# Performance work log

Hardware: AMD Instinct MI355X
Metric: run time of the kernel (lower is better)

The kernel has to match this reference:

```python
import jax, jax.numpy as jnp
import numpy as np
import math

V, D, H, KVH, L, T, B = 32000, 1024, 16, 4, 4, 2048, 2
HD = D // H            # head_dim = 64
GROUP = H // KVH       # GQA group size = 4
KVW = KVH * HD         # kv width = 256
EPS = 1e-5


def _alibi_slopes(n_heads):
    # n_heads=16 is a power of two
    start = 2.0 ** (-2.0 ** (-(math.log2(n_heads) - 3)))
    return np.array([start * start ** i for i in range(n_heads)], dtype=np.float32)


def setup_inputs() -> dict:
    key = jax.random.key(0)
    ks = jax.random.split(key, 8)
    s = 0.02
    inp = {
        "tok_emb": jax.random.normal(ks[0], (V, D), jnp.float32) * s,
        "ln1_s": jnp.ones((L, D), jnp.float32),
        "ln1_b": jnp.zeros((L, D), jnp.float32),
        "qkv_w": jax.random.normal(ks[1], (L, D, D + 2 * KVW), jnp.float32) * s,
        "qkv_b": jnp.zeros((L, D + 2 * KVW), jnp.float32),
        "proj_w": jax.random.normal(ks[2], (L, D, D), jnp.float32) * s,
        "proj_b": jnp.zeros((L, D), jnp.float32),
        "ln2_s": jnp.ones((L, D), jnp.float32),
        "ln2_b": jnp.zeros((L, D), jnp.float32),
        "fc1_w": jax.random.normal(ks[3], (L, D, 4 * D), jnp.float32) * s,
        "fc1_b": jnp.zeros((L, 4 * D), jnp.float32),
        "fc2_w": jax.random.normal(ks[4], (L, 4 * D, D), jnp.float32) * s,
        "fc2_b": jnp.zeros((L, D), jnp.float32),
        "lnf_s": jnp.ones((D,), jnp.float32),
        "lnf_b": jnp.zeros((D,), jnp.float32),
        "idx": jax.random.randint(ks[5], (B, T), 0, V, jnp.int32),
    }
    return inp


def _ln(x, s, b):
    mu = jnp.mean(x, axis=-1, keepdims=True)
    var = jnp.var(x, axis=-1, keepdims=True)
    return (x - mu) * jax.lax.rsqrt(var + EPS) * s + b


def _forward(tok_emb, ln1_s, ln1_b, qkv_w, qkv_b, proj_w, proj_b,
             ln2_s, ln2_b, fc1_w, fc1_b, fc2_w, fc2_b, lnf_s, lnf_b, idx):
    x = tok_emb[idx]  # (B, T, D); ALiBi => no learned positional embedding

    # combined causal mask + ALiBi bias: (1, H, T, T)
    slopes = jnp.asarray(_alibi_slopes(H)).reshape(1, H, 1, 1)
    pos = jnp.arange(T, dtype=jnp.float32)
    rel = jnp.minimum(pos[None, :] - pos[:, None], 0.0)  # (T, T), clamp_max(0)
    causal = pos[None, :] <= pos[:, None]
    bias = jnp.where(causal[None, None], rel[None, None] * slopes, -jnp.inf)

    scale = 1.0 / math.sqrt(HD)
    for l in range(L):
        h = _ln(x, ln1_s[l], ln1_b[l])
        qkv = h @ qkv_w[l] + qkv_b[l]
        q = qkv[..., :D].reshape(B, T, H, HD).transpose(0, 2, 1, 3)
        k = qkv[..., D:D + KVW].reshape(B, T, KVH, HD).transpose(0, 2, 1, 3)
        v = qkv[..., D + KVW:].reshape(B, T, KVH, HD).transpose(0, 2, 1, 3)
        k = jnp.repeat(k, GROUP, axis=1)  # GQA broadcast -> (B, H, T, HD)
        v = jnp.repeat(v, GROUP, axis=1)
        att = jnp.einsum("bhqd,bhkd->bhqk", q, k) * scale + bias
        att = jax.nn.softmax(att, axis=-1)
        o = jnp.einsum("bhqk,bhkd->bhqd", att, v)
        o = o.transpose(0, 2, 1, 3).reshape(B, T, D)
        x = x + o @ proj_w[l] + proj_b[l]
        h = _ln(x, ln2_s[l], ln2_b[l])
        x = x + jax.nn.gelu(h @ fc1_w[l] + fc1_b[l], approximate=False) @ fc2_w[l] + fc2_b[l]

    x = _ln(x, lnf_s, lnf_b)
    logits = x @ tok_emb.T  # tied head (no bias)
    return logits


def reference(tok_emb, ln1_s, ln1_b, qkv_w, qkv_b, proj_w, proj_b,
              ln2_s, ln2_b, fc1_w, fc1_b, fc2_w, fc2_b, lnf_s, lnf_b, idx):
    return _forward(tok_emb, ln1_s, ln1_b, qkv_w, qkv_b, proj_w, proj_b,
                    ln2_s, ln2_b, fc1_w, fc1_b, fc2_w, fc2_b, lnf_s, lnf_b, idx)
```

## Files before the change

### kernel.cpp

```cpp
#include <hip/hip_runtime.h>

#define DEV __device__ __forceinline__
typedef unsigned short u16;
typedef __bf16 bf16_t;
typedef bf16_t bf16x8 __attribute__((ext_vector_type(8)));
typedef float f32x4 __attribute__((ext_vector_type(4)));

DEV u16 f2bf(float f){ unsigned u=__float_as_uint(f); return (u16)((u + 0x7fffu + ((u>>16)&1u))>>16); }

DEV void gl_lds16(const void* g, void* l){
  __builtin_amdgcn_global_load_lds((__attribute__((address_space(1))) void*)g,
                                   (__attribute__((address_space(3))) void*)l, 16, 0, 0);
}
DEV f32x4 MFMA(bf16x8 a, bf16x8 b, f32x4 c){
  return __builtin_amdgcn_mfma_f32_16x16x32_bf16(a, b, c, 0, 0, 0);
}
DEV bf16x8 ld8(const u16* p){ return *(const bf16x8*)p; }

__global__ __launch_bounds__(256) void k_embed(const int* __restrict__ idx,
                                               const float* __restrict__ emb,
                                               float* __restrict__ x){
  int row = blockIdx.x;
  int tok = idx[row];
  const float4* s = (const float4*)(emb + (size_t)tok*1024);
  float4* d = (float4*)(x + (size_t)row*1024);
  d[threadIdx.x] = s[threadIdx.x];
}

__global__ __launch_bounds__(256) void k_ln(const float* __restrict__ x,
                                            const float* __restrict__ sc,
                                            const float* __restrict__ bi,
                                            u16* __restrict__ out){
  int row = blockIdx.x;
  const float* xr = x + (size_t)row*1024;
  float4 v = ((const float4*)xr)[threadIdx.x];
  float s = v.x+v.y+v.z+v.w;
  float q = v.x*v.x+v.y*v.y+v.z*v.z+v.w*v.w;
  #pragma unroll
  for(int m=1;m<64;m<<=1){ s += __shfl_xor(s,m); q += __shfl_xor(q,m); }
  __shared__ float ss[4], sq[4];
  int w = threadIdx.x>>6;
  if((threadIdx.x&63)==0){ ss[w]=s; sq[w]=q; }
  __syncthreads();
  s = ss[0]+ss[1]+ss[2]+ss[3];
  q = sq[0]+sq[1]+sq[2]+sq[3];
  float mu = s*(1.f/1024.f);
  float var = q*(1.f/1024.f) - mu*mu;
  float rs = rsqrtf(var + 1e-5f);
  float4 sv = ((const float4*)sc)[threadIdx.x];
  float4 bv = ((const float4*)bi)[threadIdx.x];
  ushort4 o;
  o.x = f2bf((v.x-mu)*rs*sv.x + bv.x);
  o.y = f2bf((v.y-mu)*rs*sv.y + bv.y);
  o.z = f2bf((v.z-mu)*rs*sv.z + bv.z);
  o.w = f2bf((v.w-mu)*rs*sv.w + bv.w);
  *(ushort4*)(out + (size_t)row*1024 + threadIdx.x*4) = o;
}

__global__ __launch_bounds__(256) void k_convT(const float* __restrict__ W,
                                               u16* __restrict__ Wt, int K, int N){
  __shared__ float tile[64][68];
  size_t loff = (size_t)blockIdx.z * K * N;
  W  += loff;  Wt += loff;
  int n0 = blockIdx.x*64, k0 = blockIdx.y*64;
  int tx = threadIdx.x & 15, ty = threadIdx.x >> 4;
  #pragma unroll
  for(int r=0;r<4;r++){
    int row = ty + r*16;
    float4 v = *(const float4*)&W[(size_t)(k0+row)*N + n0 + tx*4];
    *(float4*)&tile[row][tx*4] = v;
  }
  __syncthreads();
  int nn = threadIdx.x >> 2, kq = threadIdx.x & 3;
  #pragma unroll
  for(int r=0;r<4;r++){
    int k = (kq + r*4)*4;
    ushort4 o;
    o.x = f2bf(tile[k+0][nn]); o.y = f2bf(tile[k+1][nn]);
    o.z = f2bf(tile[k+2][nn]); o.w = f2bf(tile[k+3][nn]);
    *(ushort4*)&Wt[(size_t)(n0+nn)*K + k0 + k] = o;
  }
}

__global__ __launch_bounds__(256) void k_conv(const float* __restrict__ in,
                                              u16* __restrict__ out, int n4){
  int i = blockIdx.x*256 + threadIdx.x;
  if(i < n4){
    float4 v = ((const float4*)in)[i];
    ushort4 o; o.x=f2bf(v.x); o.y=f2bf(v.y); o.z=f2bf(v.z); o.w=f2bf(v.w);
    ((ushort4*)out)[i] = o;
  }
}

template<int EPI, int SWAP>
__global__ __launch_bounds__(256) void k_gemm(const u16* __restrict__ A,
                                              const u16* __restrict__ Bt,
                                              const float* __restrict__ bias,
                                              void* __restrict__ out,
                                              float* __restrict__ res,
                                              int M, int N, int K, int m_base){
  __shared__ __align__(16) u16 As[128*64];
  __shared__ __align__(16) u16 Bs[128*64];
  int t = threadIdx.x, l = t & 63, w = t >> 6;
  int g = l >> 4, lr = l & 15;
  int wr = w >> 1, wc = w & 1;
  int m0, n0;
  if constexpr(SWAP){ m0 = m_base + blockIdx.x*128; n0 = blockIdx.y*128; }
  else              { m0 = m_base + blockIdx.y*128; n0 = blockIdx.x*128; }
  f32x4 acc[4][4];
  #pragma unroll
  for(int i=0;i<4;i++)
    #pragma unroll
    for(int j=0;j<4;j++) acc[i][j] = f32x4{0.f,0.f,0.f,0.f};

  int sr = t >> 3;
  int sc = (((t & 7) ^ (sr & 7)) * 8);
  const u16* pa = A  + (size_t)(m0 + sr)*K + sc;
  const u16* pb = Bt + (size_t)(n0 + sr)*K + sc;
  u16* lda = As + t*8;
  u16* ldb = Bs + t*8;
  const int rs_a = (lr & 7)*8;

  for(int k0=0; k0<K; k0+=64){
    #pragma unroll
    for(int i=0;i<4;i++){
      gl_lds16(pa + (size_t)(i*32)*K, lda + i*2048);
      gl_lds16(pb + (size_t)(i*32)*K, ldb + i*2048);
    }
    pa += 64; pb += 64;
    __syncthreads();
    bf16x8 af[4][2], bfr[4][2];
    #pragma unroll
    for(int mi=0;mi<4;mi++){
      int row = wr*64 + mi*16 + lr;
      af[mi][0] = ld8(&As[row*64 + ((g*8     ) ^ rs_a)]);
      af[mi][1] = ld8(&As[row*64 + ((g*8 + 32) ^ rs_a)]);
    }
    #pragma unroll
    for(int ni=0;ni<4;ni++){
      int row = wc*64 + ni*16 + lr;
      bfr[ni][0] = ld8(&Bs[row*64 + ((g*8     ) ^ rs_a)]);
      bfr[ni][1] = ld8(&Bs[row*64 + ((g*8 + 32) ^ rs_a)]);
    }
    #pragma unroll
    for(int mi=0;mi<4;mi++)
      #pragma unroll
      for(int ni=0;ni<4;ni++){
        acc[mi][ni] = MFMA(af[mi][0], bfr[ni][0], acc[mi][ni]);
        acc[mi][ni] = MFMA(af[mi][1], bfr[ni][1], acc[mi][ni]);
      }
    __syncthreads();
  }

  float bv[4];
  #pragma unroll
  for(int ni=0;ni<4;ni++){
    if constexpr(EPI==3) bv[ni] = 0.f;
    else bv[ni] = bias[n0 + wc*64 + ni*16 + lr];
  }
  #pragma unroll
  for(int mi=0;mi<4;mi++){
    int row = m0 + wr*64 + mi*16 + g*4;
    #pragma unroll
    for(int ni=0;ni<4;ni++){
      int col = n0 + wc*64 + ni*16 + lr;
      #pragma unroll
      for(int r=0;r<4;r++){
        float v = acc[mi][ni][r] + bv[ni];
        size_t oidx = (size_t)(row + r)*N + col;
        if constexpr(EPI==0){
          ((u16*)out)[oidx] = f2bf(v);
        } else if constexpr(EPI==1){
          res[oidx] += v;
        } else if constexpr(EPI==2){
          float gv = 0.5f*v*(1.f + erff(v*0.70710678118654752f));
          ((u16*)out)[oidx] = f2bf(gv);
        } else {
          ((float*)out)[oidx] = v;
        }
      }
    }
  }
}

__global__ __launch_bounds__(256) void k_gemm_n64(const u16* __restrict__ A,
                                                  const u16* __restrict__ Bt,
                                                  const float* __restrict__ bias,
                                                  float* __restrict__ res,
                                                  int M, int N, int K){
  __shared__ __align__(16) u16 As[128*64];
  __shared__ __align__(16) u16 Bs[64*64];
  int t = threadIdx.x, l = t & 63, w = t >> 6;
  int g = l >> 4, lr = l & 15;
  int wr = w >> 1, wc = w & 1;
  int m0 = blockIdx.y*128, n0 = blockIdx.x*64;
  f32x4 acc[4][2];
  #pragma unroll
  for(int i=0;i<4;i++)
    #pragma unroll
    for(int j=0;j<2;j++) acc[i][j] = f32x4{0.f,0.f,0.f,0.f};

  int sr = t >> 3;
  int sc = (((t & 7) ^ (sr & 7)) * 8);
  const u16* pa = A  + (size_t)(m0 + sr)*K + sc;
  const u16* pb = Bt + (size_t)(n0 + sr)*K + sc;
  u16* lda = As + t*8;
  u16* ldb = Bs + t*8;
  const int rs_a = (lr & 7)*8;

  for(int k0=0; k0<K; k0+=64){
    #pragma unroll
    for(int i=0;i<4;i++)
      gl_lds16(pa + (size_t)(i*32)*K, lda + i*2048);
    #pragma unroll
    for(int i=0;i<2;i++)
      gl_lds16(pb + (size_t)(i*32)*K, ldb + i*2048);
    pa += 64; pb += 64;
    __syncthreads();
    bf16x8 af[4][2], bfr[2][2];
    #pragma unroll
    for(int mi=0;mi<4;mi++){
      int row = wr*64 + mi*16 + lr;
      af[mi][0] = ld8(&As[row*64 + ((g*8     ) ^ rs_a)]);
      af[mi][1] = ld8(&As[row*64 + ((g*8 + 32) ^ rs_a)]);
    }
    #pragma unroll
    for(int ni=0;ni<2;ni++){
      int row = wc*32 + ni*16 + lr;
      bfr[ni][0] = ld8(&Bs[row*64 + ((g*8     ) ^ rs_a)]);
      bfr[ni][1] = ld8(&Bs[row*64 + ((g*8 + 32) ^ rs_a)]);
    }
    #pragma unroll
    for(int mi=0;mi<4;mi++)
      #pragma unroll
      for(int ni=0;ni<2;ni++){
        acc[mi][ni] = MFMA(af[mi][0], bfr[ni][0], acc[mi][ni]);
        acc[mi][ni] = MFMA(af[mi][1], bfr[ni][1], acc[mi][ni]);
      }
    __syncthreads();
  }

  float bv[2];
  #pragma unroll
  for(int ni=0;ni<2;ni++) bv[ni] = bias[n0 + wc*32 + ni*16 + lr];
  #pragma unroll
  for(int mi=0;mi<4;mi++){
    int row = m0 + wr*64 + mi*16 + g*4;
    #pragma unroll
    for(int ni=0;ni<2;ni++){
      int col = n0 + wc*32 + ni*16 + lr;
      #pragma unroll
      for(int r=0;r<4;r++)
        res[(size_t)(row + r)*N + col] += acc[mi][ni][r] + bv[ni];
    }
  }
}

__global__ __launch_bounds__(512) void k_gemm256(const u16* __restrict__ A,
                                                 const u16* __restrict__ Bt,
                                                 float* __restrict__ out,
                                                 int M, int N, int K, int m_base){
  __shared__ __align__(16) u16 As[2][256*64];
  __shared__ __align__(16) u16 Bs[2][256*64];
  int t = threadIdx.x, l = t & 63, wid = t >> 6;
  int g = l >> 4, lr = l & 15;
  int m0 = m_base + blockIdx.x*256, n0 = blockIdx.y*256;
  f32x4 acc[2][16];
  #pragma unroll
  for(int mi=0;mi<2;mi++)
    #pragma unroll
    for(int i=0;i<16;i++) acc[mi][i] = f32x4{0.f,0.f,0.f,0.f};

  int srow = t >> 3;
  int scol = ((t & 7) ^ (srow & 7)) * 8;
  const int rs = (lr & 7) * 8;
  int nt = K >> 6;

  auto stage_half = [&](int jj, int h){
    int buf = jj & 1; int k0s = jj << 6;
    if(h < 2){
      #pragma unroll
      for(int c=0;c<2;c++){
        int rr = h*128 + c*64 + srow;
        gl_lds16(A + (size_t)(m0 + rr)*K + k0s + scol,
                 &As[buf][rr*64 + (t&7)*8]);
      }
    } else {
      #pragma unroll
      for(int c=0;c<2;c++){
        int rr = (h-2)*128 + c*64 + srow;
        gl_lds16(Bt + (size_t)(n0 + rr)*K + k0s + scol,
                 &Bs[buf][rr*64 + (t&7)*8]);
      }
    }
  };

  stage_half(0,0); stage_half(0,1); stage_half(0,2); stage_half(0,3);
  asm volatile("s_waitcnt vmcnt(2)" ::: "memory");
  __builtin_amdgcn_s_barrier();
  __builtin_amdgcn_sched_barrier(0);

  bf16x8 af[2][2];
  for(int j=0; j<nt; ++j){
    const u16* Ab = As[j & 1];
    const u16* Bb = Bs[j & 1];
    bool pf = (j + 1 < nt);
    #pragma unroll
    for(int q=0; q<4; ++q){
      if(q == 0){
        #pragma unroll
        for(int mi=0;mi<2;mi++){
          int row = wid*32 + mi*16 + lr;
          af[mi][0] = ld8(&Ab[row*64 + ((g*8     ) ^ rs)]);
          af[mi][1] = ld8(&Ab[row*64 + ((g*8 + 32) ^ rs)]);
        }
      }
      bf16x8 bfr[4][2];
      #pragma unroll
      for(int i=0;i<4;i++){
        int row = (q*4 + i)*16 + lr;
        bfr[i][0] = ld8(&Bb[row*64 + ((g*8     ) ^ rs)]);
        bfr[i][1] = ld8(&Bb[row*64 + ((g*8 + 32) ^ rs)]);
      }
      if(pf) stage_half(j+1, q);
      __builtin_amdgcn_s_barrier();
      __builtin_amdgcn_sched_barrier(0);
      __builtin_amdgcn_s_setprio(1);
      #pragma unroll
      for(int mi=0;mi<2;mi++)
        #pragma unroll
        for(int i=0;i<4;i++){
          acc[mi][q*4+i] = MFMA(af[mi][0], bfr[i][0], acc[mi][q*4+i]);
          acc[mi][q*4+i] = MFMA(af[mi][1], bfr[i][1], acc[mi][q*4+i]);
        }
      __builtin_amdgcn_s_setprio(0);
      if(q == 1) asm volatile("s_waitcnt vmcnt(4)" ::: "memory");
      if(q == 3) asm volatile("s_waitcnt vmcnt(2)" ::: "memory");
      __builtin_amdgcn_s_barrier();
      __builtin_amdgcn_sched_barrier(0);
    }
  }

  #pragma unroll
  for(int mi=0;mi<2;mi++){
    int row = m0 + wid*32 + mi*16 + g*4;
    #pragma unroll
    for(int i=0;i<16;i++){
      int col = n0 + i*16 + lr;
      #pragma unroll
      for(int r=0;r<4;r++)
        out[(size_t)(row + r)*N + col] = acc[mi][i][r];
    }
  }
}

__global__ __launch_bounds__(256) void k_gemm_f32b(const u16* __restrict__ A,
                                                   const float* __restrict__ B,
                                                   float* __restrict__ out,
                                                   int M, int N, int K, int m_base){
  __shared__ __align__(16) u16 As[128*32];
  __shared__ __align__(16) u16 Bs[128*32];
  int t = threadIdx.x, l = t & 63, w = t >> 6;
  int g = l >> 4, lr = l & 15;
  int wr = w >> 1, wc = w & 1;
  int m0 = m_base + blockIdx.y*128, n0 = blockIdx.x*128;
  f32x4 acc[4][4];
  #pragma unroll
  for(int i=0;i<4;i++)
    #pragma unroll
    for(int j=0;j<4;j++) acc[i][j] = f32x4{0.f,0.f,0.f,0.f};

  int r0 = t >> 2, c0 = (t & 3)*8;
  const u16* pa0 = A + (size_t)(m0 + r0)*K + c0;
  const u16* pa1 = A + (size_t)(m0 + r0 + 64)*K + c0;
  u16* la0 = As + t*8;  u16* la1 = As + (t+256)*8;
  int br = t >> 1, bc = (t & 1)*16;
  const float* pb = B + (size_t)(n0 + br)*K + bc;

  for(int k0=0; k0<K; k0+=32){
    gl_lds16(pa0, la0); gl_lds16(pa1, la1);
    pa0 += 32; pa1 += 32;
    float4 f0 = ((const float4*)pb)[0];
    float4 f1 = ((const float4*)pb)[1];
    float4 f2 = ((const float4*)pb)[2];
    float4 f3 = ((const float4*)pb)[3];
    pb += 32;
    ushort4 u0{f2bf(f0.x),f2bf(f0.y),f2bf(f0.z),f2bf(f0.w)};
    ushort4 u1{f2bf(f1.x),f2bf(f1.y),f2bf(f1.z),f2bf(f1.w)};
    ushort4 u2{f2bf(f2.x),f2bf(f2.y),f2bf(f2.z),f2bf(f2.w)};
    ushort4 u3{f2bf(f3.x),f2bf(f3.y),f2bf(f3.z),f2bf(f3.w)};
    *(ushort4*)&Bs[br*32 + bc +  0] = u0;
    *(ushort4*)&Bs[br*32 + bc +  4] = u1;
    *(ushort4*)&Bs[br*32 + bc +  8] = u2;
    *(ushort4*)&Bs[br*32 + bc + 12] = u3;
    __syncthreads();
    bf16x8 af[4], bfr[4];
    #pragma unroll
    for(int mi=0;mi<4;mi++) af[mi]  = ld8(&As[(wr*64 + mi*16 + lr)*32 + g*8]);
    #pragma unroll
    for(int ni=0;ni<4;ni++) bfr[ni] = ld8(&Bs[(wc*64 + ni*16 + lr)*32 + g*8]);
    #pragma unroll
    for(int mi=0;mi<4;mi++)
      #pragma unroll
      for(int ni=0;ni<4;ni++)
        acc[mi][ni] = MFMA(af[mi], bfr[ni], acc[mi][ni]);
    __syncthreads();
  }

  #pragma unroll
  for(int mi=0;mi<4;mi++){
    int row = m0 + wr*64 + mi*16 + g*4;
    #pragma unroll
    for(int ni=0;ni<4;ni++){
      int col = n0 + wc*64 + ni*16 + lr;
      #pragma unroll
      for(int r=0;r<4;r++)
        out[(size_t)(row + r)*N + col] = acc[mi][ni][r];
    }
  }
}

__global__ __launch_bounds__(512) void k_attn(const u16* __restrict__ qkv,
                                              u16* __restrict__ atto){
  __shared__ __align__(16) u16 Ksm[64*72];
  __shared__ __align__(16) u16 Vsm[64*72];
  __shared__ __align__(16) u16 Psm[8][16*72];
  int t = threadIdx.x, l = t & 63, w = t >> 6, g = l >> 4, lr = l & 15;
  int bh = blockIdx.y; int b = bh >> 4, h = bh & 15, kvh = h >> 2;
  int qb = blockIdx.x * 128;
  const float L2E = 1.44269504088896f;
  const float C1  = 0.125f * L2E;
  float slopeL = exp2f(-0.5f*(float)(h+1)) * L2E;
  float sLkt[4];
  #pragma unroll
  for(int kt=0;kt<4;kt++) sLkt[kt] = slopeL*(float)(kt*16+lr);

  int qrow = qb + w*16 + lr;
  const u16* qp = qkv + (size_t)(b*2048 + qrow)*1536 + h*64;
  bf16x8 qf0 = ld8(qp + g*8);
  bf16x8 qf1 = ld8(qp + 32 + g*8);

  bf16_t onev = (bf16_t)1.0f;
  bf16x8 onesb = {onev,onev,onev,onev,onev,onev,onev,onev};

  f32x4 oacc[4];
  #pragma unroll
  for(int i=0;i<4;i++) oacc[i] = f32x4{0.f,0.f,0.f,0.f};
  f32x4 lsum = f32x4{0.f,0.f,0.f,0.f};

  int qmax_w = qb + w*16 + 15;
  int nkb = blockIdx.x*2 + 2;
  for(int kb=0; kb<nkb; kb++){
    __syncthreads();
    {
      int key = t >> 3, ho = (t & 7)*8;
      const u16* src = qkv + (size_t)(b*2048 + kb*64 + key)*1536 + 1024 + kvh*64 + ho;
      *(int4*)&Ksm[key*72 + ho] = *(const int4*)src;
    }
    if(t < 256){
      int key0 = (t>>3)*2, hd0 = (t&7)*8;
      const u16* v0 = qkv + (size_t)(b*2048 + kb*64 + key0)*1536 + 1280 + kvh*64 + hd0;
      int4 A0 = *(const int4*)v0;
      int4 A1 = *(const int4*)(v0 + 1536);
      const u16* ua = (const u16*)&A0; const u16* ub = (const u16*)&A1;
      #pragma unroll
      for(int j=0;j<8;j++){
        int row = hd0 + j;
        int colp = key0 ^ ((row>>3)*8);
        unsigned pr = (unsigned)ua[j] | ((unsigned)ub[j]<<16);
        *(unsigned*)&Vsm[row*72 + colp] = pr;
      }
    }
    __syncthreads();
    if(kb*64 > qmax_w) continue;
    f32x4 sacc[4];
    #pragma unroll
    for(int kt=0;kt<4;kt++) sacc[kt] = f32x4{0.f,0.f,0.f,0.f};
    #pragma unroll
    for(int kt=0;kt<4;kt++){
      bf16x8 kf0 = ld8(&Ksm[(kt*16+lr)*72 + g*8]);
      bf16x8 kf1 = ld8(&Ksm[(kt*16+lr)*72 + 32 + g*8]);
      sacc[kt] = MFMA(qf0, kf0, sacc[kt]);
      sacc[kt] = MFMA(qf1, kf1, sacc[kt]);
    }
    #pragma unroll
    for(int r=0;r<4;r++){
      int q = qb + w*16 + g*4 + r;
      float base = slopeL*(float)(kb*64 - q) - 8.0f*L2E;
      #pragma unroll
      for(int kt=0;kt<4;kt++){
        int key = kb*64 + kt*16 + lr;
        float f = fmaf(sacc[kt][r], C1, base + sLkt[kt]);
        float p = (key <= q) ? exp2f(f) : 0.f;
        Psm[w][(g*4+r)*72 + kt*16 + lr] = f2bf(p);
      }
    }
    #pragma unroll
    for(int ks=0;ks<2;ks++){
      bf16x8 pf = ld8(&Psm[w][lr*72 + ks*32 + g*8]);
      lsum = MFMA(pf, onesb, lsum);
      #pragma unroll
      for(int ht=0;ht<4;ht++){
        int row = ht*16 + lr;
        int colp = (ks*32 + g*8) ^ ((row>>3)*8);
        bf16x8 vf = ld8(&Vsm[row*72 + colp]);
        oacc[ht] = MFMA(pf, vf, oacc[ht]);
      }
    }
  }
  #pragma unroll
  for(int ht=0;ht<4;ht++){
    #pragma unroll
    for(int r=0;r<4;r++){
      float o = oacc[ht][r] / lsum[r];
      atto[(size_t)(b*2048 + qb + w*16 + g*4 + r)*1024 + h*64 + ht*16 + lr] = f2bf(o);
    }
  }
}

extern "C" void kernel_launch(void* const* d_in, const int* in_sizes, int n_in,
                              void* d_out, int out_size, void* d_ws, size_t ws_size,
                              hipStream_t stream) {
  const float* tok_emb = (const float*)d_in[0];
  const float* ln1_s   = (const float*)d_in[1];
  const float* ln1_b   = (const float*)d_in[2];
  const float* qkv_w   = (const float*)d_in[3];
  const float* qkv_b   = (const float*)d_in[4];
  const float* proj_w  = (const float*)d_in[5];
  const float* proj_b  = (const float*)d_in[6];
  const float* ln2_s   = (const float*)d_in[7];
  const float* ln2_b   = (const float*)d_in[8];
  const float* fc1_w   = (const float*)d_in[9];
  const float* fc1_b   = (const float*)d_in[10];
  const float* fc2_w   = (const float*)d_in[11];
  const float* fc2_b   = (const float*)d_in[12];
  const float* lnf_s   = (const float*)d_in[13];
  const float* lnf_b   = (const float*)d_in[14];
  const int*   idx     = (const int*)d_in[15];

  char* ob = (char*)d_out;
  float* xf32  = (float*)(ob);
  u16* qkv_bf  = (u16*)(ob + (size_t)16777216);
  u16* atto_bf = (u16*)(ob + (size_t)29360128);
  u16* mid_bf  = (u16*)(ob + (size_t)37748736);
  u16* wt_qkv  = (u16*)(ob + (size_t)71303168);
  u16* wt_proj = (u16*)(ob + (size_t)83886080);
  u16* wt_fc1  = (u16*)(ob + (size_t)92274688);
  u16* wt_fc2  = (u16*)(ob + (size_t)125829120);
  u16* h_bf    = (u16*)d_ws;
  float* out   = (float*)d_out;

  bool big_ws = ws_size >= (size_t)(8388608 + 65536000);
  u16* te_bf = big_ws ? (u16*)((char*)d_ws + 8388608)
                      : (u16*)(ob + (size_t)294912000);

  k_conv<<<32000, 256, 0, stream>>>(tok_emb, te_bf, 8192000);
  k_embed<<<4096, 256, 0, stream>>>(idx, tok_emb, xf32);
  k_convT<<<dim3(24,16,4), 256, 0, stream>>>(qkv_w,  wt_qkv, 1024, 1536);
  k_convT<<<dim3(16,16,4), 256, 0, stream>>>(proj_w, wt_proj, 1024, 1024);
  k_convT<<<dim3(64,16,4), 256, 0, stream>>>(fc1_w, wt_fc1, 1024, 4096);
  k_convT<<<dim3(16,64,4), 256, 0, stream>>>(fc2_w, wt_fc2, 4096, 1024);

  for(int l=0; l<4; l++){
    k_ln<<<4096, 256, 0, stream>>>(xf32, ln1_s + (size_t)l*1024, ln1_b + (size_t)l*1024, h_bf);
    k_gemm<0,0><<<dim3(12,32), 256, 0, stream>>>(h_bf, wt_qkv + (size_t)l*1536*1024,
                                                 qkv_b + (size_t)l*1536,
                                                 qkv_bf, nullptr, 4096, 1536, 1024, 0);
    k_attn<<<dim3(16,32), 512, 0, stream>>>(qkv_bf, atto_bf);
    k_gemm_n64<<<dim3(16,32), 256, 0, stream>>>(atto_bf, wt_proj + (size_t)l*1024*1024,
                                                proj_b + (size_t)l*1024,
                                                xf32, 4096, 1024, 1024);
    k_ln<<<4096, 256, 0, stream>>>(xf32, ln2_s + (size_t)l*1024, ln2_b + (size_t)l*1024, h_bf);
    k_gemm<2,0><<<dim3(32,32), 256, 0, stream>>>(h_bf, wt_fc1 + (size_t)l*4096*1024,
                                                 fc1_b + (size_t)l*4096,
                                                 mid_bf, nullptr, 4096, 4096, 1024, 0);
    k_gemm_n64<<<dim3(16,32), 256, 0, stream>>>(mid_bf, wt_fc2 + (size_t)l*1024*4096,
                                                fc2_b + (size_t)l*1024,
                                                xf32, 4096, 1024, 4096);
  }
  k_ln<<<4096, 256, 0, stream>>>(xf32, lnf_s, lnf_b, h_bf);

  if(big_ws){
    k_gemm256<<<dim3(16,125), 512, 0, stream>>>(h_bf, te_bf, out,
                                                4096, 32000, 1024, 0);
  } else {
    k_gemm256<<<dim3(9,125), 512, 0, stream>>>(h_bf, te_bf, out,
                                               4096, 32000, 1024, 0);
    k_gemm256<<<dim3(5,125), 512, 0, stream>>>(h_bf, te_bf, out,
                                               4096, 32000, 1024, 2816);
    k_gemm_f32b<<<dim3(250,4), 256, 0, stream>>>(h_bf, tok_emb, out,
                                                 4096, 32000, 1024, 2304);
  }
}
```

Measured before the change: 1.593 ms.

## Merge embed/convert kernels, use 128x64 GEMM for QKV, skip causal mask on full blocks

Merges the token-embedding conversion and the embedding gather into one launch, which saves a kernel launch. The QKV projection now runs on the 128x64-tile GEMM variant with a new bf16 store epilogue, giving 768 workgroups instead of 384 for better occupancy on the many CUs. The attention kernel adds a fast path that skips per-element causal masking for key blocks lying fully below the diagonal. Each change is small, but together they touch launch overhead, tile shape and inner-loop ALU work.

```diff
diff --git a/kernel.cpp b/kernel.cpp
--- a/kernel.cpp
+++ b/kernel.cpp
@@ -17,14 +17,22 @@
 }
 DEV bf16x8 ld8(const u16* p){ return *(const bf16x8*)p; }
 
-__global__ __launch_bounds__(256) void k_embed(const int* __restrict__ idx,
-                                               const float* __restrict__ emb,
-                                               float* __restrict__ x){
-  int row = blockIdx.x;
-  int tok = idx[row];
-  const float4* s = (const float4*)(emb + (size_t)tok*1024);
-  float4* d = (float4*)(x + (size_t)row*1024);
-  d[threadIdx.x] = s[threadIdx.x];
+__global__ __launch_bounds__(256) void k_prep(const float* __restrict__ emb,
+                                              u16* __restrict__ te,
+                                              const int* __restrict__ idx,
+                                              float* __restrict__ x){
+  int b = blockIdx.x;
+  if(b < 32000){
+    int i = b*256 + threadIdx.x;
+    float4 v = ((const float4*)emb)[i];
+    ushort4 o; o.x=f2bf(v.x); o.y=f2bf(v.y); o.z=f2bf(v.z); o.w=f2bf(v.w);
+    ((ushort4*)te)[i] = o;
+  } else {
+    int row = b - 32000;
+    int tok = idx[row];
+    ((float4*)(x + (size_t)row*1024))[threadIdx.x] =
+        ((const float4*)(emb + (size_t)tok*1024))[threadIdx.x];
+  }
 }
 
 __global__ __launch_bounds__(256) void k_ln(const float* __restrict__ x,
@@ -82,16 +90,6 @@
   }
 }
 
-__global__ __launch_bounds__(256) void k_conv(const float* __restrict__ in,
-                                              u16* __restrict__ out, int n4){
-  int i = blockIdx.x*256 + threadIdx.x;
-  if(i < n4){
-    float4 v = ((const float4*)in)[i];
-    ushort4 o; o.x=f2bf(v.x); o.y=f2bf(v.y); o.z=f2bf(v.z); o.w=f2bf(v.w);
-    ((ushort4*)out)[i] = o;
-  }
-}
-
 template<int EPI, int SWAP>
 __global__ __launch_bounds__(256) void k_gemm(const u16* __restrict__ A,
                                               const u16* __restrict__ Bt,
@@ -183,9 +181,11 @@
   }
 }
 
+template<int EPI>
 __global__ __launch_bounds__(256) void k_gemm_n64(const u16* __restrict__ A,
                                                   const u16* __restrict__ Bt,
                                                   const float* __restrict__ bias,
+                                                  void* __restrict__ outp,
                                                   float* __restrict__ res,
                                                   int M, int N, int K){
   __shared__ __align__(16) u16 As[128*64];
@@ -250,8 +250,13 @@
     for(int ni=0;ni<2;ni++){
       int col = n0 + wc*32 + ni*16 + lr;
       #pragma unroll
-      for(int r=0;r<4;r++)
-        res[(size_t)(row + r)*N + col] += acc[mi][ni][r] + bv[ni];
+      for(int r=0;r<4;r++){
+        float v = acc[mi][ni][r] + bv[ni];
+        if constexpr(EPI==0)
+          ((u16*)outp)[(size_t)(row + r)*N + col] = f2bf(v);
+        else
+          res[(size_t)(row + r)*N + col] += v;
+      }
     }
   }
 }
@@ -448,7 +453,8 @@
   for(int i=0;i<4;i++) oacc[i] = f32x4{0.f,0.f,0.f,0.f};
   f32x4 lsum = f32x4{0.f,0.f,0.f,0.f};
 
-  int qmax_w = qb + w*16 + 15;
+  int qmin_w = qb + w*16;
+  int qmax_w = qmin_w + 15;
   int nkb = blockIdx.x*2 + 2;
   for(int kb=0; kb<nkb; kb++){
     __syncthreads();
@@ -483,16 +489,29 @@
       sacc[kt] = MFMA(qf0, kf0, sacc[kt]);
       sacc[kt] = MFMA(qf1, kf1, sacc[kt]);
     }
-    #pragma unroll
-    for(int r=0;r<4;r++){
-      int q = qb + w*16 + g*4 + r;
-      float base = slopeL*(float)(kb*64 - q) - 8.0f*L2E;
-      #pragma unroll
-      for(int kt=0;kt<4;kt++){
-        int key = kb*64 + kt*16 + lr;
-        float f = fmaf(sacc[kt][r], C1, base + sLkt[kt]);
-        float p = (key <= q) ? exp2f(f) : 0.f;
-        Psm[w][(g*4+r)*72 + kt*16 + lr] = f2bf(p);
+    if(kb*64 + 63 <= qmin_w){
+      #pragma unroll
+      for(int r=0;r<4;r++){
+        int q = qb + w*16 + g*4 + r;
+        float base = slopeL*(float)(kb*64 - q) - 8.0f*L2E;
+        #pragma unroll
+        for(int kt=0;kt<4;kt++){
+          float f = fmaf(sacc[kt][r], C1, base + sLkt[kt]);
+          Psm[w][(g*4+r)*72 + kt*16 + lr] = f2bf(exp2f(f));
+        }
+      }
+    } else {
+      #pragma unroll
+      for(int r=0;r<4;r++){
+        int q = qb + w*16 + g*4 + r;
+        float base = slopeL*(float)(kb*64 - q) - 8.0f*L2E;
+        #pragma unroll
+        for(int kt=0;kt<4;kt++){
+          int key = kb*64 + kt*16 + lr;
+          float f = fmaf(sacc[kt][r], C1, base + sLkt[kt]);
+          float p = (key <= q) ? exp2f(f) : 0.f;
+          Psm[w][(g*4+r)*72 + kt*16 + lr] = f2bf(p);
+        }
       }
     }
     #pragma unroll
@@ -554,8 +573,7 @@
   u16* te_bf = big_ws ? (u16*)((char*)d_ws + 8388608)
                       : (u16*)(ob + (size_t)294912000);
 
-  k_conv<<<32000, 256, 0, stream>>>(tok_emb, te_bf, 8192000);
-  k_embed<<<4096, 256, 0, stream>>>(idx, tok_emb, xf32);
+  k_prep<<<36096, 256, 0, stream>>>(tok_emb, te_bf, idx, xf32);
   k_convT<<<dim3(24,16,4), 256, 0, stream>>>(qkv_w,  wt_qkv, 1024, 1536);
   k_convT<<<dim3(16,16,4), 256, 0, stream>>>(proj_w, wt_proj, 1024, 1024);
   k_convT<<<dim3(64,16,4), 256, 0, stream>>>(fc1_w, wt_fc1, 1024, 4096);
@@ -563,20 +581,20 @@
 
   for(int l=0; l<4; l++){
     k_ln<<<4096, 256, 0, stream>>>(xf32, ln1_s + (size_t)l*1024, ln1_b + (size_t)l*1024, h_bf);
-    k_gemm<0,0><<<dim3(12,32), 256, 0, stream>>>(h_bf, wt_qkv + (size_t)l*1536*1024,
-                                                 qkv_b + (size_t)l*1536,
-                                                 qkv_bf, nullptr, 4096, 1536, 1024, 0);
+    k_gemm_n64<0><<<dim3(24,32), 256, 0, stream>>>(h_bf, wt_qkv + (size_t)l*1536*1024,
+                                                   qkv_b + (size_t)l*1536,
+                                                   qkv_bf, nullptr, 4096, 1536, 1024);
     k_attn<<<dim3(16,32), 512, 0, stream>>>(qkv_bf, atto_bf);
-    k_gemm_n64<<<dim3(16,32), 256, 0, stream>>>(atto_bf, wt_proj + (size_t)l*1024*1024,
-                                                proj_b + (size_t)l*1024,
-                                                xf32, 4096, 1024, 1024);
+    k_gemm_n64<1><<<dim3(16,32), 256, 0, stream>>>(atto_bf, wt_proj + (size_t)l*1024*1024,
+                                                   proj_b + (size_t)l*1024,
+                                                   nullptr, xf32, 4096, 1024, 1024);
     k_ln<<<4096, 256, 0, stream>>>(xf32, ln2_s + (size_t)l*1024, ln2_b + (size_t)l*1024, h_bf);
     k_gemm<2,0><<<dim3(32,32), 256, 0, stream>>>(h_bf, wt_fc1 + (size_t)l*4096*1024,
                                                  fc1_b + (size_t)l*4096,
                                                  mid_bf, nullptr, 4096, 4096, 1024, 0);
-    k_gemm_n64<<<dim3(16,32), 256, 0, stream>>>(mid_bf, wt_fc2 + (size_t)l*1024*4096,
-                                                fc2_b + (size_t)l*1024,
-                                                xf32, 4096, 1024, 4096);
+    k_gemm_n64<1><<<dim3(16,32), 256, 0, stream>>>(mid_bf, wt_fc2 + (size_t)l*1024*4096,
+                                                   fc2_b + (size_t)l*1024,
+                                                   nullptr, xf32, 4096, 1024, 4096);
   }
   k_ln<<<4096, 256, 0, stream>>>(xf32, lnf_s, lnf_b, h_bf);
 
```

After: 1.554 ms, median of 2. -2.4%, faster.
